# Kernel optimization log

Hardware: AMD Instinct MI355X
Metric: run time of the kernel (lower is better)

Reference implementation:

```python
import jax, jax.numpy as jnp
import numpy as np

B, N = 32, 512
NFEAT, NHID, NCLASS, NHEADS = 128, 64, 128, 8
WORK_D, SUB_D = 32, 32
H1, H2, OUT_D = 256, 256, 512
ALPHA = 0.2
NEG = -9e15


def setup_inputs() -> dict:
    key = jax.random.key(0)
    ks = jax.random.split(key, 16)
    return {
        "graph_inf": jax.random.normal(ks[0], (B, N, NFEAT), jnp.float32),
        "graph_matrix": jax.random.randint(ks[1], (B, N, N), 0, 2, jnp.int32),
        "masks": jnp.ones((B, N), jnp.float32),
        "node_order": jax.random.randint(ks[2], (B,), 0, N, jnp.int64),
        "work": jax.random.normal(ks[3], (B, WORK_D), jnp.float32),
        "subtask": jax.random.normal(ks[4], (B, SUB_D), jnp.float32),
        # GAT head params
        "W_heads": jax.random.normal(ks[5], (NHEADS, NFEAT, NHID), jnp.float32) * 0.1,
        "a_heads": jax.random.normal(ks[6], (NHEADS, 2 * NHID), jnp.float32) * 0.1,
        "W_out": jax.random.normal(ks[7], (NHID * NHEADS, NCLASS), jnp.float32) * 0.05,
        "a_out": jax.random.normal(ks[8], (2 * NCLASS,), jnp.float32) * 0.1,
        # MLP encoder params
        "fc1_w": jax.random.normal(ks[9], (NCLASS + WORK_D + SUB_D, H1), jnp.float32) * 0.07,
        "fc1_b": jnp.zeros((H1,), jnp.float32),
        "fc2_w": jax.random.normal(ks[10], (H1, H2), jnp.float32) * 0.06,
        "fc2_b": jnp.zeros((H2,), jnp.float32),
        "fc3_w": jax.random.normal(ks[11], (H2, OUT_D), jnp.float32) * 0.06,
        "fc3_b": jnp.zeros((OUT_D,), jnp.float32),
    }


def _gat_layer(Wh, a1, a2, adj, masks):
    # Wh: [B,N,F]; additive GAT score e_ij = leakyrelu(a1.Wh_i + a2.Wh_j)
    s1 = Wh @ a1  # [B,N]
    s2 = Wh @ a2  # [B,N]
    e = jax.nn.leaky_relu(s1[:, :, None] + s2[:, None, :], ALPHA)  # [B,N,N]
    att = jax.nn.softmax(jnp.where(adj > 0, e, NEG), axis=2)
    h_prime = jnp.einsum('bnm,bmf->bnf', att, Wh)
    return h_prime * masks[:, :, None]


def reference(graph_inf, graph_matrix, masks, node_order, work, subtask,
              W_heads, a_heads, W_out, a_out,
              fc1_w, fc1_b, fc2_w, fc2_b, fc3_w, fc3_b):
    adj = graph_matrix
    # multi-head GAT layer (concat=True -> ELU)
    def head(Wk, ak):
        Wh = jnp.einsum('bnf,fo->bno', graph_inf, Wk)
        return jax.nn.elu(_gat_layer(Wh, ak[:NHID], ak[NHID:], adj, masks))
    xh = jax.vmap(head)(W_heads, a_heads)  # [H,B,N,NHID]
    x = jnp.transpose(xh, (1, 2, 0, 3)).reshape(B, N, NHEADS * NHID)
    # output GAT layer (concat=False)
    Wh = jnp.einsum('bnf,fo->bno', x, W_out)
    x = _gat_layer(Wh, a_out[:NCLASS], a_out[NCLASS:], adj, masks)
    x = x * masks[:, :, None]
    # select subtask node per batch element
    selected = x[jnp.arange(B), node_order]  # [B,NCLASS]
    inf = jnp.concatenate([selected, work, subtask], axis=1)
    h = jax.nn.relu(inf @ fc1_w + fc1_b)
    h = jax.nn.relu(h @ fc2_w + fc2_b)
    out = h @ fc3_w + fc3_b
    return jax.nn.softmax(out, axis=-1)
```

## Files before the change

### kernel.cpp

```cpp
#include <hip/hip_runtime.h>

typedef unsigned short u16;
typedef unsigned int u32;
typedef unsigned long long u64;

typedef __bf16 bf16x8 __attribute__((ext_vector_type(8)));
typedef float f32x4 __attribute__((ext_vector_type(4)));

#define LOG2E 1.44269504088896340736f

__device__ __forceinline__ float b2f(u16 u) {
    u32 x = ((u32)u) << 16;
    return __builtin_bit_cast(float, x);
}
__device__ __forceinline__ u16 f2b(float f) {
    u32 u = __builtin_bit_cast(u32, f);
    u32 r = (u + 0x7fffu + ((u >> 16) & 1u)) >> 16;
    return (u16)r;
}
__device__ __forceinline__ float ld(const void* p, int i, bool bf) {
    return bf ? b2f(((const u16*)p)[i]) : ((const float*)p)[i];
}
__device__ __forceinline__ bool detect_bf16(const void* masks) {
    return ((const u16*)masks)[0] != 0;
}
__device__ __forceinline__ f32x4 mfma16(bf16x8 a, bf16x8 b, f32x4 c) {
    return __builtin_amdgcn_mfma_f32_16x16x32_bf16(a, b, c, 0, 0, 0);
}

__device__ __attribute__((aligned(256))) u32  g_adjm[16384 * 16];
__device__ __attribute__((aligned(256))) u16  g_BT1[512 * 128];
__device__ __attribute__((aligned(256))) u16  g_BT2[128 * 512];
__device__ __attribute__((aligned(256))) u16  g_Xc[32 * 512 * 128];
__device__ __attribute__((aligned(256))) u16  g_Wh1[512 * 16384];
__device__ __attribute__((aligned(256))) u16  g_xb[16384 * 512];
__device__ __attribute__((aligned(256))) u16  g_Wh2[16384 * 128];
__device__ __attribute__((aligned(256))) float g_s1a[131072];
__device__ __attribute__((aligned(256))) float g_s2a[131072];
__device__ __attribute__((aligned(256))) float g_s1b[16384];
__device__ __attribute__((aligned(256))) float g_s2b[16384];
__device__ __attribute__((aligned(256))) u16  g_fc1T[256 * 192];
__device__ __attribute__((aligned(256))) u16  g_fc2T[256 * 256];
__device__ __attribute__((aligned(256))) u16  g_fc3T[512 * 256];
__device__ __attribute__((aligned(256))) u16  g_Ahi[32 * 192];
__device__ __attribute__((aligned(256))) u16  g_Alo[32 * 192];
__device__ __attribute__((aligned(256))) u16  g_H1hi[32 * 256];
__device__ __attribute__((aligned(256))) u16  g_H1lo[32 * 256];
__device__ __attribute__((aligned(256))) u16  g_H2hi[32 * 256];
__device__ __attribute__((aligned(256))) u16  g_H2lo[32 * 256];
__device__ __attribute__((aligned(256))) float g_logits[32 * 512];

__global__ __launch_bounds__(256) void prep_kernel(
    const int* __restrict__ adj, const void* __restrict__ Whd,
    const void* __restrict__ Wo, const void* __restrict__ Xin,
    const void* __restrict__ fc1w, const void* __restrict__ fc2w,
    const void* __restrict__ fc3w, const void* __restrict__ masks)
{
    const bool bf = detect_bf16(masks);
    const int blk = blockIdx.x;
    const int tid = threadIdx.x;
    if (blk < 1024) {
        int id = blk * 256 + tid;
        int row = id >> 4, w = id & 15;
        const int4* p = (const int4*)(adj + row * 512 + w * 32);
        int4 v[8];
        #pragma unroll
        for (int s = 0; s < 8; ++s) v[s] = p[s];
        u32 word = 0;
        #pragma unroll
        for (int s = 0; s < 8; ++s) {
            u32 nib = (v[s].x > 0 ? 1u : 0u) | (v[s].y > 0 ? 2u : 0u) |
                      (v[s].z > 0 ? 4u : 0u) | (v[s].w > 0 ? 8u : 0u);
            word |= nib << (4 * s);
        }
        g_adjm[id] = word;
    } else if (blk < 1028) {
        int base = (blk - 1024) * 16384;
        for (int e = base + tid; e < base + 16384; e += 256) {
            int n = e >> 7, k = e & 127;
            g_BT1[e] = f2b(ld(Whd, (n >> 6) * 8192 + k * 64 + (n & 63), bf));
        }
    } else if (blk < 1032) {
        int base = (blk - 1028) * 16384;
        for (int e = base + tid; e < base + 16384; e += 256) {
            int n = e >> 9, k = e & 511;
            g_BT2[e] = f2b(ld(Wo, k * 128 + n, bf));
        }
    } else if (blk < 1288) {
        if (!bf) {
            int base = (blk - 1032) * 8192;
            for (int e = base + tid; e < base + 8192; e += 256)
                g_Xc[e] = f2b(((const float*)Xin)[e]);
        }
    } else if (blk < 1294) {
        int base = (blk - 1288) * 8192;
        for (int e = base + tid; e < base + 8192; e += 256) {
            int n = e / 192, k = e - n * 192;
            g_fc1T[e] = f2b(ld(fc1w, k * 256 + n, bf));
        }
    } else if (blk < 1302) {
        int base = (blk - 1294) * 8192;
        for (int e = base + tid; e < base + 8192; e += 256) {
            int n = e >> 8, k = e & 255;
            g_fc2T[e] = f2b(ld(fc2w, k * 256 + n, bf));
        }
    } else {
        int base = (blk - 1302) * 8192;
        for (int e = base + tid; e < base + 8192; e += 256) {
            int n = e >> 8, k = e & 255;
            g_fc3T[e] = f2b(ld(fc3w, k * 512 + n, bf));
        }
    }
}

__global__ __launch_bounds__(256, 2) void gemm1_kernel(
    const void* __restrict__ Xin, const void* __restrict__ a_heads,
    const void* __restrict__ masks)
{
    __shared__ __attribute__((aligned(16))) u16 Asl[128 * 72];
    __shared__ __attribute__((aligned(16))) u16 Bsl[128 * 72];
    const bool bf = detect_bf16(masks);
    const u16* Bsrc = bf ? (const u16*)Xin : g_Xc;
    const int tid = threadIdx.x;
    const int wave = tid >> 6, lane = tid & 63;
    const int wr = wave >> 1, wc = wave & 1;
    const int c = lane & 15, q = lane >> 4;
    const int tm = blockIdx.x * 128, tn = blockIdx.y * 128;
    const int srow = tid >> 1, sh = (tid & 1) * 32;
    f32x4 acc[4][4] = {};
    for (int kc = 0; kc < 128; kc += 64) {
        __syncthreads();
        const u16* Ag = g_BT1 + (tm + srow) * 128 + kc + sh;
        const u16* Bg = Bsrc + (tn + srow) * 128 + kc + sh;
        #pragma unroll
        for (int s = 0; s < 4; ++s) {
            *(uint4*)&Asl[srow * 72 + sh + 8 * s] = *(const uint4*)(Ag + 8 * s);
            *(uint4*)&Bsl[srow * 72 + sh + 8 * s] = *(const uint4*)(Bg + 8 * s);
        }
        __syncthreads();
        #pragma unroll
        for (int kt = 0; kt < 2; ++kt) {
            bf16x8 af[4], bfr[4];
            #pragma unroll
            for (int rt = 0; rt < 4; ++rt)
                af[rt] = *(const bf16x8*)&Asl[(wr * 64 + rt * 16 + c) * 72 + kt * 32 + q * 8];
            #pragma unroll
            for (int ct = 0; ct < 4; ++ct)
                bfr[ct] = *(const bf16x8*)&Bsl[(wc * 64 + ct * 16 + c) * 72 + kt * 32 + q * 8];
            #pragma unroll
            for (int rt = 0; rt < 4; ++rt)
                #pragma unroll
                for (int ct = 0; ct < 4; ++ct)
                    acc[rt][ct] = mfma16(af[rt], bfr[ct], acc[rt][ct]);
        }
    }
    #pragma unroll
    for (int rt = 0; rt < 4; ++rt)
        #pragma unroll
        for (int ct = 0; ct < 4; ++ct)
            #pragma unroll
            for (int i = 0; i < 4; ++i) {
                int r = tm + wr * 64 + rt * 16 + q * 4 + i;
                int col = tn + wc * 64 + ct * 16 + c;
                g_Wh1[r * 16384 + col] = f2b(acc[rt][ct][i]);
            }
    const int hh = blockIdx.x * 2 + wr;
    const int b = tn >> 9;
    const int nbase = (tn & 511) + wc * 64;
    float a1v[4][4], a2v[4][4];
    #pragma unroll
    for (int rt = 0; rt < 4; ++rt)
        #pragma unroll
        for (int i = 0; i < 4; ++i) {
            int o = rt * 16 + q * 4 + i;
            a1v[rt][i] = ld(a_heads, hh * 128 + o, bf);
            a2v[rt][i] = ld(a_heads, hh * 128 + 64 + o, bf);
        }
    #pragma unroll
    for (int ct = 0; ct < 4; ++ct) {
        float p1 = 0.f, p2 = 0.f;
        #pragma unroll
        for (int rt = 0; rt < 4; ++rt)
            #pragma unroll
            for (int i = 0; i < 4; ++i) {
                p1 += acc[rt][ct][i] * a1v[rt][i];
                p2 += acc[rt][ct][i] * a2v[rt][i];
            }
        p1 += __shfl_xor(p1, 16); p1 += __shfl_xor(p1, 32);
        p2 += __shfl_xor(p2, 16); p2 += __shfl_xor(p2, 32);
        if (lane < 16) {
            int n = nbase + ct * 16 + lane;
            g_s1a[(b * 8 + hh) * 512 + n] = p1 * LOG2E;
            g_s2a[(b * 8 + hh) * 512 + n] = p2 * LOG2E;
        }
    }
}

__global__ __launch_bounds__(256, 4) void att1_kernel(const void* __restrict__ masks)
{
    __shared__ float s1s[128];
    __shared__ float s2s[512];

    const bool bf = detect_bf16(masks);
    const int tid = threadIdx.x;
    const int w = tid >> 6, lane = tid & 63;
    const int c = lane & 15, q = lane >> 4;
    const int q4 = blockIdx.x & 3;
    const int h  = (blockIdx.x >> 2) & 7;
    const int b  = blockIdx.x >> 5;

    s2s[tid]       = g_s2a[(b * 8 + h) * 512 + tid];
    s2s[tid + 256] = g_s2a[(b * 8 + h) * 512 + 256 + tid];
    if (tid < 128) s1s[tid] = g_s1a[(b * 8 + h) * 512 + q4 * 128 + tid];
    __syncthreads();

    const u32* adjb = g_adjm + b * 8192;
    const u16* wt = g_Wh1 + (u32)(h * 64) * 16384 + b * 512;

    const u32 bword = (c == 0) ? 0x3F803F80u : 0u;
    const uint4 bq = {bword, bword, bword, bword};
    const bf16x8 bone = __builtin_bit_cast(bf16x8, bq);

    f32x4 acc[2][4] = {};
    f32x4 acc1[2] = {};
    const int row0 = q4 * 128 + w * 16 + c;
    const int row1 = row0 + 64;
    const float s1v0 = s1s[w * 16 + c];
    const float s1v1 = s1s[64 + w * 16 + c];

    for (int kc = 0; kc < 4; ++kc) {
        union { uint4 v; u32 a[4]; } wq0, wq1;
        wq0.v = *(const uint4*)(adjb + row0 * 16 + kc * 4);
        wq1.v = *(const uint4*)(adjb + row1 * 16 + kc * 4);
        #pragma unroll
        for (int tl = 0; tl < 4; ++tl) {
            union { float4 v[2]; float f[8]; } s2r;
            s2r.v[0] = *(const float4*)&s2s[kc * 128 + tl * 32 + q * 8];
            s2r.v[1] = *(const float4*)&s2s[kc * 128 + tl * 32 + q * 8 + 4];
            bf16x8 bfrag[4];
            #pragma unroll
            for (int nt = 0; nt < 4; ++nt)
                bfrag[nt] = *(const bf16x8*)(wt + (u32)(nt * 16 + c) * 16384 +
                                             kc * 128 + tl * 32 + q * 8);
            #pragma unroll
            for (int g = 0; g < 2; ++g) {
                const float s1v = g ? s1v1 : s1v0;
                u32 wbits = (g ? wq1.a[tl] : wq0.a[tl]) >> (q * 8);
                u32 pk[4];
                #pragma unroll
                for (int pi = 0; pi < 4; ++pi) {
                    float e0 = s1v + s2r.f[2 * pi];
                    float e1 = s1v + s2r.f[2 * pi + 1];
                    e0 = fmaxf(e0, 0.2f * e0);
                    e1 = fmaxf(e1, 0.2f * e1);
                    u32 u0 = __builtin_bit_cast(u32, exp2f(e0));
                    u32 u1 = __builtin_bit_cast(u32, exp2f(e1));
                    u0 = ((wbits >> (2 * pi)) & 1u) ? u0 : 0u;
                    u1 = ((wbits >> (2 * pi + 1)) & 1u) ? u1 : 0u;
                    pk[pi] = __builtin_amdgcn_perm(u1, u0, 0x07060302u);
                }
                uint4 pkv = {pk[0], pk[1], pk[2], pk[3]};
                bf16x8 pv = __builtin_bit_cast(bf16x8, pkv);
                acc1[g] = mfma16(pv, bone, acc1[g]);
                #pragma unroll
                for (int nt = 0; nt < 4; ++nt)
                    acc[g][nt] = mfma16(pv, bfrag[nt], acc[g][nt]);
            }
        }
    }
    #pragma unroll
    for (int g = 0; g < 2; ++g) {
        const int R = q4 * 128 + g * 64 + w * 16;
        #pragma unroll
        for (int i = 0; i < 4; ++i) {
            float lr = __shfl(acc1[g][i], (lane & 48));
            float invr = (lr == 0.f) ? (1.f / 512.f) : (1.f / lr);
            const int row = R + q * 4 + i;
            float mk = ld(masks, b * 512 + row, bf);
            #pragma unroll
            for (int nt = 0; nt < 4; ++nt) {
                float v = acc[g][nt][i] * invr * mk;
                float o = v > 0.f ? v : (__expf(v) - 1.f);
                g_xb[(b * 512 + row) * 512 + h * 64 + nt * 16 + c] = f2b(o);
            }
        }
    }
}

__global__ __launch_bounds__(256, 2) void gemm2_kernel(
    const void* __restrict__ a_out, const void* __restrict__ masks)
{
    __shared__ __attribute__((aligned(16))) u16 Asl[64 * 72];
    __shared__ __attribute__((aligned(16))) u16 Bsl[128 * 72];
    const int tid = threadIdx.x;
    const int w = tid >> 6, lane = tid & 63;
    const int c = lane & 15, q = lane >> 4;
    const int tm = blockIdx.x * 64;
    const int rowA = tid >> 2, shA = (tid & 3) * 16;
    const int rowB = tid >> 1, shB = (tid & 1) * 32;
    f32x4 acc[8] = {};
    for (int kc = 0; kc < 512; kc += 64) {
        __syncthreads();
        const u16* Ag = g_xb + (tm + rowA) * 512 + kc + shA;
        *(uint4*)&Asl[rowA * 72 + shA] = *(const uint4*)Ag;
        *(uint4*)&Asl[rowA * 72 + shA + 8] = *(const uint4*)(Ag + 8);
        const u16* Bg = g_BT2 + rowB * 512 + kc + shB;
        #pragma unroll
        for (int s = 0; s < 4; ++s)
            *(uint4*)&Bsl[rowB * 72 + shB + 8 * s] = *(const uint4*)(Bg + 8 * s);
        __syncthreads();
        #pragma unroll
        for (int kt = 0; kt < 2; ++kt) {
            bf16x8 av = *(const bf16x8*)&Asl[(w * 16 + c) * 72 + kt * 32 + q * 8];
            #pragma unroll
            for (int ct = 0; ct < 8; ++ct) {
                bf16x8 bv = *(const bf16x8*)&Bsl[(ct * 16 + c) * 72 + kt * 32 + q * 8];
                acc[ct] = mfma16(av, bv, acc[ct]);
            }
        }
    }
    const bool bf = detect_bf16(masks);
    float a1v[8], a2v[8];
    #pragma unroll
    for (int ct = 0; ct < 8; ++ct) {
        a1v[ct] = ld(a_out, ct * 16 + c, bf);
        a2v[ct] = ld(a_out, 128 + ct * 16 + c, bf);
    }
    #pragma unroll
    for (int i = 0; i < 4; ++i) {
        float p1 = 0.f, p2 = 0.f;
        #pragma unroll
        for (int ct = 0; ct < 8; ++ct) {
            p1 += acc[ct][i] * a1v[ct];
            p2 += acc[ct][i] * a2v[ct];
        }
        #pragma unroll
        for (int off = 1; off < 16; off <<= 1) {
            p1 += __shfl_xor(p1, off);
            p2 += __shfl_xor(p2, off);
        }
        if (c == 0) {
            int m = tm + w * 16 + q * 4 + i;
            g_s1b[m] = p1 * LOG2E;
            g_s2b[m] = p2 * LOG2E;
        }
    }
    #pragma unroll
    for (int ct = 0; ct < 8; ++ct)
        #pragma unroll
        for (int i = 0; i < 4; ++i) {
            int m = tm + w * 16 + q * 4 + i;
            g_Wh2[m * 128 + ct * 16 + c] = f2b(acc[ct][i]);
        }
}

__global__ __launch_bounds__(256) void fin_att(
    const void* __restrict__ masks, const int* __restrict__ node_order,
    const void* __restrict__ workv, const void* __restrict__ subtaskv)
{
    __shared__ float att[512];
    __shared__ float parts[16][128];
    __shared__ float redl[4];

    const bool bf = detect_bf16(masks);
    const int b = blockIdx.x, t = threadIdx.x;
    const int lane = t & 63, wv = t >> 6;
    const int istar = node_order[b];

    const float s1v = g_s1b[b * 512 + istar];
    const u32* arow = g_adjm + (b * 512 + istar) * 16;
    float ssum = 0.f;
    #pragma unroll
    for (int rep = 0; rep < 2; ++rep) {
        int j = t + rep * 256;
        float e = s1v + g_s2b[b * 512 + j];
        e = fmaxf(e, 0.2f * e);
        float ex = ((arow[j >> 5] >> (j & 31)) & 1u) ? exp2f(e) : 0.f;
        att[j] = ex;
        ssum += ex;
    }
    for (int off = 1; off < 64; off <<= 1) ssum += __shfl_xor(ssum, off);
    if (lane == 0) redl[wv] = ssum;
    __syncthreads();
    float tot = redl[0] + redl[1] + redl[2] + redl[3];
    bool uni = (tot == 0.f);
    float inv = uni ? (1.f / 512.f) : (1.f / tot);

    const int og = t & 15, jg = t >> 4;
    float acc[8] = {};
    const u16* base = g_Wh2 + (b * 512 + jg * 32) * 128 + og * 8;
    #pragma unroll 8
    for (int j0 = 0; j0 < 32; ++j0) {
        float wgt = uni ? 1.f : att[jg * 32 + j0];
        union { u16 u[8]; uint4 v; } z;
        z.v = *(const uint4*)(base + j0 * 128);
        #pragma unroll
        for (int i = 0; i < 8; ++i) acc[i] += wgt * b2f(z.u[i]);
    }
    #pragma unroll
    for (int i = 0; i < 8; ++i) parts[jg][og * 8 + i] = acc[i];
    __syncthreads();
    float mk = ld(masks, b * 512 + istar, bf);
    if (t < 128) {
        float s = 0.f;
        #pragma unroll
        for (int jj = 0; jj < 16; ++jj) s += parts[jj][t];
        s *= inv * mk * mk;
        u16 hi = f2b(s);
        g_Ahi[b * 192 + t] = hi;
        g_Alo[b * 192 + t] = f2b(s - b2f(hi));
    } else if (t < 160) {
        g_Ahi[b * 192 + t] = bf ? ((const u16*)workv)[b * 32 + t - 128]
                                : f2b(((const float*)workv)[b * 32 + t - 128]);
        g_Alo[b * 192 + t] = 0;
    } else if (t < 192) {
        g_Ahi[b * 192 + t] = bf ? ((const u16*)subtaskv)[b * 32 + t - 160]
                                : f2b(((const float*)subtaskv)[b * 32 + t - 160]);
        g_Alo[b * 192 + t] = 0;
    }
}

template<int K, int NOUT, bool RELU>
__device__ __forceinline__ void mlp_body(
    const u16* __restrict__ Ahi, const u16* __restrict__ Alo,
    const u16* __restrict__ WT, const void* __restrict__ bias,
    u16* __restrict__ Ohi, u16* __restrict__ Olo, float* __restrict__ Of,
    const void* __restrict__ masks)
{
    const bool bf = detect_bf16(masks);
    const int t = threadIdx.x, w = t >> 6, lane = t & 63;
    const int c = lane & 15, q = lane >> 4;
    const int col = blockIdx.x * 64 + w * 16 + c;

    const u16* wp  = WT + col * K + q * 8;
    const u16* ahp = Ahi + c * K + q * 8;
    const u16* alp = Alo + c * K + q * 8;

    f32x4 acc0 = {}, acc1 = {};
    #pragma unroll
    for (int kt = 0; kt < K / 32; ++kt) {
        bf16x8 bw  = *(const bf16x8*)(wp + kt * 32);
        bf16x8 ah0 = *(const bf16x8*)(ahp + kt * 32);
        bf16x8 al0 = *(const bf16x8*)(alp + kt * 32);
        bf16x8 ah1 = *(const bf16x8*)(ahp + 16 * K + kt * 32);
        bf16x8 al1 = *(const bf16x8*)(alp + 16 * K + kt * 32);
        acc0 = mfma16(ah0, bw, acc0);
        acc0 = mfma16(al0, bw, acc0);
        acc1 = mfma16(ah1, bw, acc1);
        acc1 = mfma16(al1, bw, acc1);
    }
    float bs = ld(bias, col, bf);
    #pragma unroll
    for (int mt = 0; mt < 2; ++mt) {
        f32x4 a = mt ? acc1 : acc0;
        #pragma unroll
        for (int i = 0; i < 4; ++i) {
            int m = mt * 16 + q * 4 + i;
            float v = a[i] + bs;
            if (RELU) {
                v = fmaxf(v, 0.f);
                u16 hi = f2b(v);
                Ohi[m * NOUT + col] = hi;
                Olo[m * NOUT + col] = f2b(v - b2f(hi));
            } else {
                Of[m * NOUT + col] = v;
            }
        }
    }
}

__global__ __launch_bounds__(256) void mlp1_kernel(const void* bias, const void* masks) {
    mlp_body<192, 256, true>(g_Ahi, g_Alo, g_fc1T, bias, g_H1hi, g_H1lo, nullptr, masks);
}
__global__ __launch_bounds__(256) void mlp2_kernel(const void* bias, const void* masks) {
    mlp_body<256, 256, true>(g_H1hi, g_H1lo, g_fc2T, bias, g_H2hi, g_H2lo, nullptr, masks);
}
__global__ __launch_bounds__(256) void mlp3_kernel(const void* bias, const void* masks) {
    mlp_body<256, 512, false>(g_H2hi, g_H2lo, g_fc3T, bias, nullptr, nullptr, g_logits, masks);
}

__global__ __launch_bounds__(64) void softmax_kernel(
    const void* __restrict__ masks, void* __restrict__ out)
{
    const bool bf = detect_bf16(masks);
    const int row = blockIdx.x, lane = threadIdx.x;
    const float* lp = g_logits + row * 512 + lane * 8;
    float v[8];
    *(float4*)&v[0] = *(const float4*)lp;
    *(float4*)&v[4] = *(const float4*)(lp + 4);
    float mx = v[0];
    #pragma unroll
    for (int i = 1; i < 8; ++i) mx = fmaxf(mx, v[i]);
    for (int off = 1; off < 64; off <<= 1) mx = fmaxf(mx, __shfl_xor(mx, off));
    float e[8];
    float s = 0.f;
    #pragma unroll
    for (int i = 0; i < 8; ++i) { e[i] = __expf(v[i] - mx); s += e[i]; }
    for (int off = 1; off < 64; off <<= 1) s += __shfl_xor(s, off);
    float inv = 1.f / s;
    if (bf) {
        u16* o = (u16*)out + row * 512 + lane * 8;
        #pragma unroll
        for (int i = 0; i < 8; ++i) o[i] = f2b(e[i] * inv);
    } else {
        float* o = (float*)out + row * 512 + lane * 8;
        #pragma unroll
        for (int i = 0; i < 8; ++i) o[i] = e[i] * inv;
    }
}

extern "C" void kernel_launch(void* const* d_in, const int* in_sizes, int n_in,
                              void* d_out, int out_size, void* d_ws, size_t ws_size,
                              hipStream_t stream)
{
    const void* graph_inf    = d_in[0];
    const int*  graph_matrix = (const int*)d_in[1];
    const void* masks        = d_in[2];
    const int*  node_order   = (const int*)d_in[3];
    const void* work         = d_in[4];
    const void* subtask      = d_in[5];
    const void* W_heads      = d_in[6];
    const void* a_heads      = d_in[7];
    const void* W_out        = d_in[8];
    const void* a_out        = d_in[9];
    const void* fc1w         = d_in[10];
    const void* fc1b         = d_in[11];
    const void* fc2w         = d_in[12];
    const void* fc2b         = d_in[13];
    const void* fc3w         = d_in[14];
    const void* fc3b         = d_in[15];

    prep_kernel<<<dim3(1318), dim3(256), 0, stream>>>(graph_matrix, W_heads, W_out, graph_inf,
                                                      fc1w, fc2w, fc3w, masks);
    gemm1_kernel<<<dim3(4, 128), dim3(256), 0, stream>>>(graph_inf, a_heads, masks);
    att1_kernel<<<dim3(1024), dim3(256), 0, stream>>>(masks);
    gemm2_kernel<<<dim3(256), dim3(256), 0, stream>>>(a_out, masks);
    fin_att<<<dim3(32), dim3(256), 0, stream>>>(masks, node_order, work, subtask);
    mlp1_kernel<<<dim3(4), dim3(256), 0, stream>>>(fc1b, masks);
    mlp2_kernel<<<dim3(4), dim3(256), 0, stream>>>(fc2b, masks);
    mlp3_kernel<<<dim3(8), dim3(256), 0, stream>>>(fc3b, masks);
    softmax_kernel<<<dim3(32), dim3(64), 0, stream>>>(masks, d_out);
}
```

Before: 206.3 us.

## Factor GAT attention exp into per-row and per-column exponentials

The attention kernel now precomputes exp2(s2) and exp2(0.2*s2) per column in shared memory and exp2(s1), exp2(0.2*s1) per row. Each score becomes a product E1*E2 and selects the leaky branch by comparing the product against 1, replacing one transcendental per element with two multiplies. Blocks are enlarged to 1024 threads covering all 512 rows of a (batch, head) pair, which cuts the grid to 256 blocks and removes redundant s2 loads. The product form can overflow or underflow where the direct exp would not, and the bigger blocks lower scheduling flexibility and occupancy per CU.

After: 206.8 us. No clear change (+0.2%).

```diff
diff --git a/kernel.cpp b/kernel.cpp
--- a/kernel.cpp
+++ b/kernel.cpp
@@ -196,22 +196,24 @@
     }
 }
 
-__global__ __launch_bounds__(256, 4) void att1_kernel(const void* __restrict__ masks)
-{
-    __shared__ float s1s[128];
-    __shared__ float s2s[512];
+__global__ __launch_bounds__(1024, 1) void att1_kernel(const void* __restrict__ masks)
+{
+    __shared__ float E2s[512];
+    __shared__ float E2ps[512];
 
     const bool bf = detect_bf16(masks);
     const int tid = threadIdx.x;
     const int w = tid >> 6, lane = tid & 63;
     const int c = lane & 15, q = lane >> 4;
-    const int q4 = blockIdx.x & 3;
-    const int h  = (blockIdx.x >> 2) & 7;
-    const int b  = blockIdx.x >> 5;
-
-    s2s[tid]       = g_s2a[(b * 8 + h) * 512 + tid];
-    s2s[tid + 256] = g_s2a[(b * 8 + h) * 512 + 256 + tid];
-    if (tid < 128) s1s[tid] = g_s1a[(b * 8 + h) * 512 + q4 * 128 + tid];
+    const int h  = blockIdx.x & 7;
+    const int b  = blockIdx.x >> 3;
+
+    {
+        int j = tid & 511;
+        float s2v = g_s2a[(b * 8 + h) * 512 + j];
+        if (tid < 512) E2s[j] = exp2f(s2v);
+        else           E2ps[j] = exp2f(0.2f * s2v);
+    }
     __syncthreads();
 
     const u32* adjb = g_adjm + b * 8192;
@@ -221,12 +223,15 @@
     const uint4 bq = {bword, bword, bword, bword};
     const bf16x8 bone = __builtin_bit_cast(bf16x8, bq);
 
+    const int row0 = w * 32 + c;
+    const int row1 = row0 + 16;
+    const float s1r0 = g_s1a[(b * 8 + h) * 512 + row0];
+    const float s1r1 = g_s1a[(b * 8 + h) * 512 + row1];
+    const float E1_0 = exp2f(s1r0), E1p_0 = exp2f(0.2f * s1r0);
+    const float E1_1 = exp2f(s1r1), E1p_1 = exp2f(0.2f * s1r1);
+
     f32x4 acc[2][4] = {};
     f32x4 acc1[2] = {};
-    const int row0 = q4 * 128 + w * 16 + c;
-    const int row1 = row0 + 64;
-    const float s1v0 = s1s[w * 16 + c];
-    const float s1v1 = s1s[64 + w * 16 + c];
 
     for (int kc = 0; kc < 4; ++kc) {
         union { uint4 v; u32 a[4]; } wq0, wq1;
@@ -234,30 +239,35 @@
         wq1.v = *(const uint4*)(adjb + row1 * 16 + kc * 4);
         #pragma unroll
         for (int tl = 0; tl < 4; ++tl) {
-            union { float4 v[2]; float f[8]; } s2r;
-            s2r.v[0] = *(const float4*)&s2s[kc * 128 + tl * 32 + q * 8];
-            s2r.v[1] = *(const float4*)&s2s[kc * 128 + tl * 32 + q * 8 + 4];
+            const int base = kc * 128 + tl * 32 + q * 8;
+            union { float4 v[2]; float f[8]; } e2r, e2pr;
+            e2r.v[0]  = *(const float4*)&E2s[base];
+            e2r.v[1]  = *(const float4*)&E2s[base + 4];
+            e2pr.v[0] = *(const float4*)&E2ps[base];
+            e2pr.v[1] = *(const float4*)&E2ps[base + 4];
             bf16x8 bfrag[4];
             #pragma unroll
             for (int nt = 0; nt < 4; ++nt)
-                bfrag[nt] = *(const bf16x8*)(wt + (u32)(nt * 16 + c) * 16384 +
-                                             kc * 128 + tl * 32 + q * 8);
+                bfrag[nt] = *(const bf16x8*)(wt + (u32)(nt * 16 + c) * 16384 + base);
             #pragma unroll
             for (int g = 0; g < 2; ++g) {
-                const float s1v = g ? s1v1 : s1v0;
+                const float E1  = g ? E1_1  : E1_0;
+                const float E1p = g ? E1p_1 : E1p_0;
                 u32 wbits = (g ? wq1.a[tl] : wq0.a[tl]) >> (q * 8);
                 u32 pk[4];
                 #pragma unroll
                 for (int pi = 0; pi < 4; ++pi) {
-                    float e0 = s1v + s2r.f[2 * pi];
-                    float e1 = s1v + s2r.f[2 * pi + 1];
-                    e0 = fmaxf(e0, 0.2f * e0);
-                    e1 = fmaxf(e1, 0.2f * e1);
-                    u32 u0 = __builtin_bit_cast(u32, exp2f(e0));
-                    u32 u1 = __builtin_bit_cast(u32, exp2f(e1));
-                    u0 = ((wbits >> (2 * pi)) & 1u) ? u0 : 0u;
-                    u1 = ((wbits >> (2 * pi + 1)) & 1u) ? u1 : 0u;
-                    pk[pi] = __builtin_amdgcn_perm(u1, u0, 0x07060302u);
+                    float p0  = E1 * e2r.f[2 * pi];
+                    float pp0 = E1p * e2pr.f[2 * pi];
+                    float z0 = p0 > 1.f ? p0 : pp0;
+                    z0 = ((wbits >> (2 * pi)) & 1u) ? z0 : 0.f;
+                    float p1  = E1 * e2r.f[2 * pi + 1];
+                    float pp1 = E1p * e2pr.f[2 * pi + 1];
+                    float z1 = p1 > 1.f ? p1 : pp1;
+                    z1 = ((wbits >> (2 * pi + 1)) & 1u) ? z1 : 0.f;
+                    pk[pi] = __builtin_amdgcn_perm(__builtin_bit_cast(u32, z1),
+                                                   __builtin_bit_cast(u32, z0),
+                                                   0x07060302u);
                 }
                 uint4 pkv = {pk[0], pk[1], pk[2], pk[3]};
                 bf16x8 pv = __builtin_bit_cast(bf16x8, pkv);
@@ -270,7 +280,7 @@
     }
     #pragma unroll
     for (int g = 0; g < 2; ++g) {
-        const int R = q4 * 128 + g * 64 + w * 16;
+        const int R = w * 32 + g * 16;
         #pragma unroll
         for (int i = 0; i < 4; ++i) {
             float lr = __shfl(acc1[g][i], (lane & 48));
@@ -533,7 +543,7 @@
     prep_kernel<<<dim3(1318), dim3(256), 0, stream>>>(graph_matrix, W_heads, W_out, graph_inf,
                                                       fc1w, fc2w, fc3w, masks);
     gemm1_kernel<<<dim3(4, 128), dim3(256), 0, stream>>>(graph_inf, a_heads, masks);
-    att1_kernel<<<dim3(1024), dim3(256), 0, stream>>>(masks);
+    att1_kernel<<<dim3(256), dim3(1024), 0, stream>>>(masks);
     gemm2_kernel<<<dim3(256), dim3(256), 0, stream>>>(a_out, masks);
     fin_att<<<dim3(32), dim3(256), 0, stream>>>(masks, node_order, work, subtask);
     mlp1_kernel<<<dim3(4), dim3(256), 0, stream>>>(fc1b, masks);
```
